# Optimization experiments

Hardware: AMD Instinct MI355X
Metric: run time of the kernel (lower is better)

## Reference

```python
import jax, jax.numpy as jnp
import numpy as np
from jax import lax

NUM_ANCHORS_PER_LEVEL = [196608, 49152, 12288, 3072, 768]
PRE_NMS_TOP_N = 1000
POST_NMS_TOP_N = 1000
NMS_THRESH = 0.7
SCORE_THRESH = 0.0
MIN_SIZE = 0.001
BBOX_XFORM_CLIP = float(np.log(1000.0 / 16.0))
NEG = -1e9


def setup_inputs() -> dict:
    key = jax.random.key(0)
    k1, k2, k3, k4 = jax.random.split(key, 4)
    B = 16
    A = sum(NUM_ANCHORS_PER_LEVEL)
    objectness = jax.random.normal(k1, (B, A), jnp.float32)
    pred_bbox_deltas = jax.random.normal(k2, (B, A, 4), jnp.float32) * 0.1
    cxcy = jax.random.uniform(k3, (A, 2), jnp.float32, 0.0, 1024.0)
    wh = jax.random.uniform(k4, (A, 2), jnp.float32, 16.0, 256.0)
    anchors = jnp.concatenate([cxcy - 0.5 * wh, cxcy + 0.5 * wh], axis=1)
    return {"objectness": objectness, "pred_bbox_deltas": pred_bbox_deltas,
            "anchors": anchors, "image_h": 1024, "image_w": 1024}


def _decode(deltas, anchors):
    # torchvision BoxCoder.decode_single with weights (1,1,1,1)
    # deltas [B, A, 4], anchors [A, 4] -> proposals [B, A, 4] (x1,y1,x2,y2)
    w = anchors[:, 2] - anchors[:, 0]
    h = anchors[:, 3] - anchors[:, 1]
    cx = anchors[:, 0] + 0.5 * w
    cy = anchors[:, 1] + 0.5 * h
    dx, dy = deltas[..., 0], deltas[..., 1]
    dw = jnp.minimum(deltas[..., 2], BBOX_XFORM_CLIP)
    dh = jnp.minimum(deltas[..., 3], BBOX_XFORM_CLIP)
    pcx = dx * w + cx
    pcy = dy * h + cy
    pw = jnp.exp(dw) * w
    ph = jnp.exp(dh) * h
    return jnp.stack([pcx - 0.5 * pw, pcy - 0.5 * ph,
                      pcx + 0.5 * pw, pcy + 0.5 * ph], axis=-1)


def _get_top_n_idx(obj):
    # per-level topk with global offsets, static level sizes -> static shapes
    r, off = [], 0
    for n in NUM_ANCHORS_PER_LEVEL:
        k = min(PRE_NMS_TOP_N, n)
        _, idx = lax.top_k(obj[:, off:off + n], k)
        r.append(idx + off)
        off += n
    return jnp.concatenate(r, axis=1)  # [B, K]


def _nms_keep(boxes, scores, valid):
    # Greedy NMS (torchvision semantics: suppress iou > thresh). Fixed-shape mask version.
    K = boxes.shape[0]
    order = jnp.argsort(-scores)
    b = boxes[order]
    v = valid[order]
    area = jnp.maximum(b[:, 2] - b[:, 0], 0.0) * jnp.maximum(b[:, 3] - b[:, 1], 0.0)
    pos = jnp.arange(K)

    def body(i, keep):
        cur = b[i]
        xx1 = jnp.maximum(cur[0], b[:, 0])
        yy1 = jnp.maximum(cur[1], b[:, 1])
        xx2 = jnp.minimum(cur[2], b[:, 2])
        yy2 = jnp.minimum(cur[3], b[:, 3])
        inter = jnp.maximum(xx2 - xx1, 0.0) * jnp.maximum(yy2 - yy1, 0.0)
        iou = inter / (area[i] + area - inter + 1e-9)
        suppress = (iou > NMS_THRESH) & (pos > i) & keep[i]
        return keep & ~suppress

    keep = lax.fori_loop(0, K, body, v)
    return jnp.zeros(K, bool).at[order].set(keep)


def _process_image(boxes, scores_logit, lvl, img_h, img_w):
    # clip_boxes_to_image
    x1 = jnp.clip(boxes[:, 0], 0.0, img_w)
    y1 = jnp.clip(boxes[:, 1], 0.0, img_h)
    x2 = jnp.clip(boxes[:, 2], 0.0, img_w)
    y2 = jnp.clip(boxes[:, 3], 0.0, img_h)
    boxes = jnp.stack([x1, y1, x2, y2], axis=-1)
    scores = jax.nn.sigmoid(scores_logit)
    ws, hs = x2 - x1, y2 - y1
    valid = (ws >= MIN_SIZE) & (hs >= MIN_SIZE) & (scores >= SCORE_THRESH)
    # batched_nms: offset boxes per level so classes never overlap
    max_coord = jnp.max(boxes)
    offs = lvl.astype(boxes.dtype) * (max_coord + 1.0)
    nms_boxes = boxes + offs[:, None]
    masked = jnp.where(valid, scores, NEG)
    keep = _nms_keep(nms_boxes, masked, valid)
    sel = jnp.where(keep, masked, NEG)
    top_s, top_i = lax.top_k(sel, POST_NMS_TOP_N)
    out_valid = top_s > NEG / 2
    fb = jnp.where(out_valid[:, None], boxes[top_i], 0.0)
    fs = jnp.where(out_valid, top_s, 0.0)
    return fb, fs


def reference(objectness, pred_bbox_deltas, anchors, image_h, image_w):
    proposals = _decode(pred_bbox_deltas, anchors)      # [B, A, 4]
    obj = lax.stop_gradient(objectness)                 # objectness.detach()
    top_idx = _get_top_n_idx(obj)                       # [B, K]
    levels_full = jnp.concatenate([jnp.full((n,), i, jnp.int32)
                                   for i, n in enumerate(NUM_ANCHORS_PER_LEVEL)])
    sel_obj = jnp.take_along_axis(obj, top_idx, axis=1)               # [B, K]
    sel_boxes = jnp.take_along_axis(proposals, top_idx[..., None], axis=1)  # [B, K, 4]
    sel_lvl = levels_full[top_idx]                                    # [B, K]
    fh, fw = float(image_h), float(image_w)
    boxes, scores = jax.vmap(lambda b, s, l: _process_image(b, s, l, fh, fw))(
        sel_boxes, sel_obj, sel_lvl)
    return boxes, scores
```

## Files before the change

### kernel.cpp

```cpp
#include <hip/hip_runtime.h>


#define A_TOTAL 261888
#define B_IMG   16
#define K_TOT   4768
#define NEGV    -1e9f
#define BBOX_CLIP 4.135166556742356f
#define ROWS    1024
#define JOBS_PER_IMG 622
#define TOTAL_JOBS   9952
#define CAPG    4096
#define SL_PER_IMG 18

__constant__ int c_lvl_off[5] = {0, 196608, 245760, 258048, 261120};
__constant__ int c_lvl_n[5]   = {196608, 49152, 12288, 3072, 768};
__constant__ int c_lvl_k[5]   = {1000, 1000, 1000, 1000, 768};
__constant__ int c_sel_off[5] = {0, 1000, 2000, 3000, 4000};

__constant__ int c_s_lvl[SL_PER_IMG]   = {0,0,0,0,0,0,0,0,0,0,0,0, 1,1,1, 2, 3, 4};
__constant__ int c_s_base4[SL_PER_IMG] = {0,4096,8192,12288,16384,20480,24576,28672,
                                          32768,36864,40960,45056, 0,4096,8192, 0, 0, 0};
__constant__ int c_s_len4[SL_PER_IMG]  = {4096,4096,4096,4096,4096,4096,4096,4096,
                                          4096,4096,4096,4096, 4096,4096,4096, 3072, 768, 192};

typedef unsigned long long ull;

__device__ __forceinline__ unsigned fkey(float f) {
    unsigned u = __float_as_uint(f);
    return (u & 0x80000000u) ? ~u : (u | 0x80000000u);
}
__device__ __forceinline__ float inv_fkey(unsigned h) {
    return (h & 0x80000000u) ? __uint_as_float(h ^ 0x80000000u)
                             : __uint_as_float(~h);
}
__device__ __forceinline__ float rlane_f(float v, int l) {
    return __int_as_float(__builtin_amdgcn_readlane(__float_as_int(v), l));
}
__device__ __forceinline__ ull rlane_u64(ull v, int l) {
    int lo = __builtin_amdgcn_readlane((int)(unsigned)v, l);
    int hi = __builtin_amdgcn_readlane((int)(unsigned)(v >> 32), l);
    return ((ull)(unsigned)hi << 32) | (unsigned)lo;
}

__device__ __forceinline__ void bitonic_desc(ull* keys, int S, int tid, int nth) {
    for (int kk = 2; kk <= S; kk <<= 1) {
        for (int jj = kk >> 1; jj > 0; jj >>= 1) {
            for (int i = tid; i < S; i += nth) {
                int ix = i ^ jj;
                if (ix > i) {
                    ull a = keys[i], c = keys[ix];
                    bool desc = ((i & kk) == 0);
                    if (desc ? (a < c) : (a > c)) { keys[i] = c; keys[ix] = a; }
                }
            }
            __syncthreads();
        }
    }
}

__global__ void __launch_bounds__(1024)
init_kernel(unsigned* __restrict__ ghist, int* __restrict__ gcnt,
            ull* __restrict__ growany) {
    const int gid = blockIdx.x * 1024 + threadIdx.x;
    if (gid < 80 * 4096) ghist[gid] = 0u;
    if (gid < 80) gcnt[gid] = 0;
    if (gid < 80 * 16) growany[gid] = 0ull;
}

__global__ void __launch_bounds__(256)
hist_kernel(const float* __restrict__ obj, unsigned* __restrict__ ghist) {
    const int blk = blockIdx.x, b = blk / SL_PER_IMG, r = blk % SL_PER_IMG;
    const int lvl = c_s_lvl[r], base4 = c_s_base4[r], len4 = c_s_len4[r];
    const int g = b * 5 + lvl;
    const int tid = threadIdx.x;
    const float4* src4 = (const float4*)(obj + (size_t)b * A_TOTAL + c_lvl_off[lvl]) + base4;

    __shared__ unsigned lh[2 * 4096];
    for (int i = tid; i < 2 * 4096; i += 256) lh[i] = 0u;
    __syncthreads();
    unsigned* myh = lh + (tid & 1) * 4096;
    for (int i = tid; i < len4; i += 256) {
        float4 v = src4[i];
        atomicAdd(&myh[fkey(v.x) >> 20], 1u);
        atomicAdd(&myh[fkey(v.y) >> 20], 1u);
        atomicAdd(&myh[fkey(v.z) >> 20], 1u);
        atomicAdd(&myh[fkey(v.w) >> 20], 1u);
    }
    __syncthreads();
    for (int bin = tid; bin < 4096; bin += 256) {
        unsigned v = lh[bin] + lh[4096 + bin];
        if (v) atomicAdd(&ghist[g * 4096 + bin], v);
    }
}

__global__ void __launch_bounds__(1024)
thresh_kernel(const unsigned* __restrict__ ghist, unsigned* __restrict__ Tg,
              int* __restrict__ flagg) {
    const int g = blockIdx.x, lvl = g % 5;
    const int n = c_lvl_n[lvl], k = c_lvl_k[lvl];
    const int tid = threadIdx.x;
    if (k >= n) {
        if (tid == 0) { Tg[g] = 0u; flagg[g] = 0; }
        return;
    }
    __shared__ unsigned csum[1024];
    __shared__ int sh_chunk;
    unsigned s = 0;
    for (int q = 0; q < 4; ++q) s += ghist[g * 4096 + tid * 4 + q];
    csum[tid] = s;
    __syncthreads();
    for (int o = 1; o < 1024; o <<= 1) {
        unsigned v = (tid + o < 1024) ? csum[tid + o] : 0u;
        __syncthreads();
        csum[tid] += v;
        __syncthreads();
    }
    if (csum[tid] >= (unsigned)k && (tid == 1023 || csum[tid + 1] < (unsigned)k))
        sh_chunk = tid;
    __syncthreads();
    if (tid == 0) {
        int I = sh_chunk;
        unsigned cum = (I < 1023) ? csum[I + 1] : 0u;
        unsigned bin = 0, cntge = 0;
        for (int c = I * 4 + 3; c >= I * 4; --c) {
            unsigned h = ghist[g * 4096 + c];
            if (cum + h >= (unsigned)k) { bin = (unsigned)c; cntge = cum + h; break; }
            cum += h;
        }
        if (cntge <= CAPG) { Tg[g] = bin << 20; flagg[g] = 0; }
        else               { Tg[g] = 0u;        flagg[g] = 1; }
    }
}

__global__ void __launch_bounds__(256)
collect_kernel(const float* __restrict__ obj, const unsigned* __restrict__ Tg,
               const int* __restrict__ flagg, ull* __restrict__ gkeys,
               int* __restrict__ gcnt) {
    const int blk = blockIdx.x, b = blk / SL_PER_IMG, r = blk % SL_PER_IMG;
    const int lvl = c_s_lvl[r], base4 = c_s_base4[r], len4 = c_s_len4[r];
    const int g = b * 5 + lvl;
    const int tid = threadIdx.x;
    if (flagg[g]) return;
    const unsigned T = Tg[g];
    const float4* src4 = (const float4*)(obj + (size_t)b * A_TOTAL + c_lvl_off[lvl]) + base4;

    __shared__ ull buf[CAPG];
    __shared__ int scnt, sbase;
    if (tid == 0) scnt = 0;
    __syncthreads();
    for (int i = tid; i < len4; i += 256) {
        float4 v = src4[i];
        unsigned u0 = fkey(v.x), u1 = fkey(v.y), u2 = fkey(v.z), u3 = fkey(v.w);
        int al = (base4 + i) << 2;
        if (u0 >= T) { int p = atomicAdd(&scnt, 1); if (p < CAPG) buf[p] = ((ull)u0 << 32) | (unsigned)(~(unsigned)(al + 0)); }
        if (u1 >= T) { int p = atomicAdd(&scnt, 1); if (p < CAPG) buf[p] = ((ull)u1 << 32) | (unsigned)(~(unsigned)(al + 1)); }
        if (u2 >= T) { int p = atomicAdd(&scnt, 1); if (p < CAPG) buf[p] = ((ull)u2 << 32) | (unsigned)(~(unsigned)(al + 2)); }
        if (u3 >= T) { int p = atomicAdd(&scnt, 1); if (p < CAPG) buf[p] = ((ull)u3 << 32) | (unsigned)(~(unsigned)(al + 3)); }
    }
    __syncthreads();
    int c2 = scnt < CAPG ? scnt : CAPG;
    if (tid == 0) sbase = atomicAdd(&gcnt[g], c2);
    __syncthreads();
    for (int j = tid; j < c2; j += 256) {
        int d = sbase + j;
        if (d < CAPG) gkeys[g * CAPG + d] = buf[j];
    }
}

__global__ void __launch_bounds__(1024)
sortgather_kernel(const float* __restrict__ obj, const float* __restrict__ deltas,
                  const float* __restrict__ anchors, const int* __restrict__ ihp,
                  const int* __restrict__ iwp, const unsigned* __restrict__ ghist,
                  const unsigned* __restrict__ Tg, const int* __restrict__ flagg,
                  const ull* __restrict__ gkeys, const int* __restrict__ gcnt,
                  float4* __restrict__ cand_box, float* __restrict__ cand_masked,
                  float* __restrict__ mclvl) {
    const int g = blockIdx.x, b = g / 5, lvl = g % 5;
    const int n = c_lvl_n[lvl], k = c_lvl_k[lvl], off = c_lvl_off[lvl];
    const int so = c_sel_off[lvl];
    const int tid = threadIdx.x;

    __shared__ ull cl[CAPG];
    __shared__ float redf[1024];
    __shared__ unsigned fhist[256];
    __shared__ unsigned csum[1024];
    __shared__ int sh_chunk, sh_rem, sh_cnt;
    __shared__ unsigned sh_bin;

    int cnt;
    if (!flagg[g]) {
        cnt = gcnt[g];
        if (cnt < 0) cnt = 0;
        if (cnt > CAPG) cnt = CAPG;
        for (int i = tid; i < cnt; i += 1024) cl[i] = gkeys[g * CAPG + i];
    } else {
        const float4* src4 = (const float4*)(obj + (size_t)b * A_TOTAL + off);
        const int n4 = n >> 2;
        unsigned s = 0;
        for (int q = 0; q < 4; ++q) s += ghist[g * 4096 + tid * 4 + q];
        csum[tid] = s;
        __syncthreads();
        for (int o = 1; o < 1024; o <<= 1) {
            unsigned v = (tid + o < 1024) ? csum[tid + o] : 0u;
            __syncthreads();
            csum[tid] += v;
            __syncthreads();
        }
        if (csum[tid] >= (unsigned)k && (tid == 1023 || csum[tid + 1] < (unsigned)k))
            sh_chunk = tid;
        __syncthreads();
        if (tid == 0) {
            int I = sh_chunk;
            unsigned cum = (I < 1023) ? csum[I + 1] : 0u;
            for (int c = I * 4 + 3; c >= I * 4; --c) {
                unsigned h = ghist[g * 4096 + c];
                if (cum + h >= (unsigned)k) { sh_bin = (unsigned)c; sh_rem = k - (int)cum; break; }
                cum += h;
            }
        }
        __syncthreads();
        unsigned prefix = sh_bin;
        int rem = sh_rem, done = 12;
        while (done < 32) {
            int w = (32 - done >= 8) ? 8 : (32 - done);
            int shift = 32 - done - w;
            int nb = 1 << w;
            for (int i = tid; i < nb; i += 1024) fhist[i] = 0u;
            __syncthreads();
            for (int i = tid; i < n4; i += 1024) {
                float4 v = src4[i];
                unsigned uu0 = fkey(v.x), uu1 = fkey(v.y), uu2 = fkey(v.z), uu3 = fkey(v.w);
                if ((uu0 >> (shift + w)) == prefix) atomicAdd(&fhist[(uu0 >> shift) & (nb - 1)], 1u);
                if ((uu1 >> (shift + w)) == prefix) atomicAdd(&fhist[(uu1 >> shift) & (nb - 1)], 1u);
                if ((uu2 >> (shift + w)) == prefix) atomicAdd(&fhist[(uu2 >> shift) & (nb - 1)], 1u);
                if ((uu3 >> (shift + w)) == prefix) atomicAdd(&fhist[(uu3 >> shift) & (nb - 1)], 1u);
            }
            __syncthreads();
            if (tid == 0) {
                unsigned cum = 0;
                for (int c = nb - 1; c >= 0; --c) {
                    unsigned h = fhist[c];
                    if (cum + h >= (unsigned)rem) {
                        sh_bin = (prefix << w) | (unsigned)c;
                        sh_rem = rem - (int)cum;
                        break;
                    }
                    cum += h;
                }
            }
            __syncthreads();
            prefix = sh_bin; rem = sh_rem; done += w;
            __syncthreads();
        }
        unsigned T = prefix;
        if (tid == 0) sh_cnt = 0;
        __syncthreads();
        for (int i = tid; i < n4; i += 1024) {
            float4 v = src4[i];
            unsigned u0 = fkey(v.x), u1 = fkey(v.y), u2 = fkey(v.z), u3 = fkey(v.w);
            int base = i << 2;
            if (u0 >= T) { int p = atomicAdd(&sh_cnt, 1); if (p < CAPG) cl[p] = ((ull)u0 << 32) | (unsigned)(~(unsigned)(base + 0)); }
            if (u1 >= T) { int p = atomicAdd(&sh_cnt, 1); if (p < CAPG) cl[p] = ((ull)u1 << 32) | (unsigned)(~(unsigned)(base + 1)); }
            if (u2 >= T) { int p = atomicAdd(&sh_cnt, 1); if (p < CAPG) cl[p] = ((ull)u2 << 32) | (unsigned)(~(unsigned)(base + 2)); }
            if (u3 >= T) { int p = atomicAdd(&sh_cnt, 1); if (p < CAPG) cl[p] = ((ull)u3 << 32) | (unsigned)(~(unsigned)(base + 3)); }
        }
        __syncthreads();
        cnt = sh_cnt; if (cnt > CAPG) cnt = CAPG;
    }

    int S = 1024; while (S < cnt) S <<= 1;
    for (int i = cnt + tid; i < S; i += 1024) cl[i] = 0ull;
    __syncthreads();
    bitonic_desc(cl, S, tid, 1024);

    const float imh = (float)ihp[0];
    const float imw = (float)iwp[0];
    float mx = 0.0f;
    if (tid < k) {
        ull kv = cl[tid];
        unsigned idx = (unsigned)off + (unsigned)(~(unsigned)kv);
        float logit = inv_fkey((unsigned)(kv >> 32));
        float4 anc = ((const float4*)anchors)[idx];
        float w = __fsub_rn(anc.z, anc.x);
        float h = __fsub_rn(anc.w, anc.y);
        float cx = __fadd_rn(anc.x, __fmul_rn(0.5f, w));
        float cy = __fadd_rn(anc.y, __fmul_rn(0.5f, h));
        float4 dl = ((const float4*)deltas)[(size_t)b * A_TOTAL + idx];
        float dx = dl.x, dy = dl.y;
        float dw = fminf(dl.z, BBOX_CLIP);
        float dh = fminf(dl.w, BBOX_CLIP);
        float pcx = __fadd_rn(__fmul_rn(dx, w), cx);
        float pcy = __fadd_rn(__fmul_rn(dy, h), cy);
        float pw = __fmul_rn(expf(dw), w);
        float ph = __fmul_rn(expf(dh), h);
        float x1 = __fsub_rn(pcx, __fmul_rn(0.5f, pw));
        float y1 = __fsub_rn(pcy, __fmul_rn(0.5f, ph));
        float x2 = __fadd_rn(pcx, __fmul_rn(0.5f, pw));
        float y2 = __fadd_rn(pcy, __fmul_rn(0.5f, ph));
        x1 = fminf(fmaxf(x1, 0.0f), imw);
        y1 = fminf(fmaxf(y1, 0.0f), imh);
        x2 = fminf(fmaxf(x2, 0.0f), imw);
        y2 = fminf(fmaxf(y2, 0.0f), imh);
        float score = 1.0f / __fadd_rn(1.0f, expf(-logit));
        bool valid = (__fsub_rn(x2, x1) >= 0.001f) && (__fsub_rn(y2, y1) >= 0.001f);
        cand_box[b * K_TOT + so + tid] = make_float4(x1, y1, x2, y2);
        cand_masked[b * K_TOT + so + tid] = valid ? score : NEGV;
        mx = fmaxf(fmaxf(x1, y1), fmaxf(x2, y2));
    }
    redf[tid] = mx;
    __syncthreads();
    for (int s2 = 512; s2 > 0; s2 >>= 1) {
        if (tid < s2) redf[tid] = fmaxf(redf[tid], redf[tid + s2]);
        __syncthreads();
    }
    if (tid == 0) mclvl[g] = redf[0];
}

__global__ void __launch_bounds__(1024)
sortprep_kernel(const float4* __restrict__ cand_box, const float* __restrict__ cand_masked,
                const float* __restrict__ mclvl,
                float4* __restrict__ sbox, float* __restrict__ sar,
                ull* __restrict__ skeys, ull* __restrict__ svalid) {
    const int g = blockIdx.x, b = g / 5, lvl = g % 5;
    const int n = c_lvl_k[lvl], so = c_sel_off[lvl];
    const int tid = threadIdx.x;
    __shared__ ull keys[1024];
    __shared__ ull sv[16];
    if (tid < 16) sv[tid] = 0ull;
    if (tid < n) {
        float m = cand_masked[b * K_TOT + so + tid];
        keys[tid] = ((ull)fkey(m) << 32) | (unsigned)(~(unsigned)(so + tid));
    } else {
        keys[tid] = 0ull;
    }
    __syncthreads();
    bitonic_desc(keys, 1024, tid, 1024);

    float mc = fmaxf(fmaxf(fmaxf(mclvl[b * 5 + 0], mclvl[b * 5 + 1]),
                           fmaxf(mclvl[b * 5 + 2], mclvl[b * 5 + 3])),
                     mclvl[b * 5 + 4]);
    const float offs = __fmul_rn((float)lvl, __fadd_rn(mc, 1.0f));
    const int r = tid;
    ull kv = keys[r];
    skeys[g * ROWS + r] = kv;
    if (r < n) {
        int slot = (int)(~(unsigned)kv);
        float4 bb = cand_box[b * K_TOT + slot];
        float X1 = __fadd_rn(bb.x, offs);
        float Y1 = __fadd_rn(bb.y, offs);
        float X2 = __fadd_rn(bb.z, offs);
        float Y2 = __fadd_rn(bb.w, offs);
        sbox[g * ROWS + r] = make_float4(X1, Y1, X2, Y2);
        sar[g * ROWS + r] = __fmul_rn(fmaxf(__fsub_rn(X2, X1), 0.0f),
                                      fmaxf(__fsub_rn(Y2, Y1), 0.0f));
        if (inv_fkey((unsigned)(kv >> 32)) <= -1e8f)
            atomicOr(&sv[r >> 6], 1ull << (r & 63));
    } else {
        sbox[g * ROWS + r] = make_float4(0.f, 0.f, 0.f, 0.f);
        sar[g * ROWS + r] = 0.f;
    }
    __syncthreads();
    if (tid < 16) svalid[g * 16 + tid] = sv[tid];
}

__global__ void __launch_bounds__(256)
maskbuild_kernel(const float4* __restrict__ sbox, const float* __restrict__ sar,
                 ull* __restrict__ maskg, ull* __restrict__ growany) {
    const int wave = (blockIdx.x * 256 + threadIdx.x) >> 6;
    const int lane = threadIdx.x & 63;
    if (wave >= TOTAL_JOBS) return;
    const int img = wave / JOBS_PER_IMG;
    int rem = wave - img * JOBS_PER_IMG;
    int lvl, t;
    if (rem >= 544) { lvl = 4; t = rem - 544; }
    else            { lvl = rem / 136; t = rem - lvl * 136; }
    const int g = img * 5 + lvl;
    const int Rp = (c_lvl_k[lvl] + 63) >> 6;
    int rt = 0, tt = t;
    while (tt >= Rp - rt) { tt -= Rp - rt; ++rt; }
    const int ct = rt + tt;
    const int r0 = rt << 6, c0 = ct << 6;

    const float4 rb = sbox[g * ROWS + r0 + lane];
    const float  ra = sar[g * ROWS + r0 + lane];
    const float4 cb = sbox[g * ROWS + c0 + lane];
    const float  ca = sar[g * ROWS + c0 + lane];
    const int row = r0 + lane;

    ull m = 0ull;
    for (int jj = 0; jj < 64; ++jj) {
        float bx1 = rlane_f(cb.x, jj);
        float by1 = rlane_f(cb.y, jj);
        float bx2 = rlane_f(cb.z, jj);
        float by2 = rlane_f(cb.w, jj);
        float aj  = rlane_f(ca, jj);
        float xx1 = fmaxf(rb.x, bx1);
        float yy1 = fmaxf(rb.y, by1);
        float xx2 = fminf(rb.z, bx2);
        float yy2 = fminf(rb.w, by2);
        float inter = __fmul_rn(fmaxf(__fsub_rn(xx2, xx1), 0.0f),
                                fmaxf(__fsub_rn(yy2, yy1), 0.0f));
        float den = __fadd_rn(__fsub_rn(__fadd_rn(ra, aj), inter), 1e-9f);
        float iou = inter / den;
        bool s = (iou > 0.7f) && (c0 + jj > row);
        m |= ((ull)s) << jj;
    }
    maskg[(size_t)(g * 16 + ct) * ROWS + row] = m;
    ull ab = __ballot(m != 0ull);
    if (lane == 0 && ab)
        atomicOr(&growany[g * 16 + rt], ab);
}

__global__ void __launch_bounds__(1024)
scan_kernel(const ull* __restrict__ maskg, const ull* __restrict__ growany,
            const ull* __restrict__ svalid, const ull* __restrict__ skeys,
            ull* __restrict__ klist, int* __restrict__ kcount) {
    const int g = blockIdx.x, lvl = g % 5;
    const int n = c_lvl_k[lvl];
    const int Rp = (n + 63) >> 6;
    const int tid = threadIdx.x;

    __shared__ ull lmask[1024 * 17];
    __shared__ ull lsk[1024];

    if (tid < n) {
        ull rw = growany[g * 16 + (tid >> 6)];
        if ((rw >> (tid & 63)) & 1ull) {
            #pragma unroll 16
            for (int w = 0; w < 16; ++w) {
                ull v = (w < Rp) ? maskg[(size_t)(g * 16 + w) * ROWS + tid] : 0ull;
                lmask[tid * 17 + w] = v;
            }
        }
        lsk[tid] = skeys[g * ROWS + tid];
    }
    __syncthreads();
    if (tid >= 16) return;

    const int lane = tid;
    ull remv_l = svalid[g * 16 + lane];
    ull rany_l = growany[g * 16 + lane];
    ull kpv = 0ull;
    for (int W = 0; W < Rp; ++W) {
        const int base = W << 6;
        const int lim = (n - base >= 64) ? 64 : (n - base);
        const ull wmask = (lim >= 64) ? ~0ull : ((1ull << lim) - 1ull);
        ull curw = rlane_u64(remv_l, W);
        ull heavy = rlane_u64(rany_l, W) & wmask;
        while (heavy) {
            const int j = __ffsll((long long)heavy) - 1;
            heavy &= heavy - 1;
            if (!((curw >> j) & 1ull)) {
                ull mrow = lmask[(base + j) * 17 + lane];
                remv_l |= mrow;
                curw |= rlane_u64(mrow, W);
            }
        }
        kpv = (lane == W) ? (~curw & wmask) : kpv;
    }

    int myc = __popcll(kpv);
    int pos = 0, tot = 0;
    for (int w2 = 0; w2 < 16; ++w2) {
        int c = __builtin_amdgcn_readlane(myc, w2);
        pos += (w2 < lane) ? c : 0;
        tot += c;
    }
    if (lane == 0) kcount[g] = tot;
    ull kw = kpv;
    while (kw) {
        int bit = __ffsll((long long)kw) - 1;
        kw &= kw - 1;
        klist[g * ROWS + pos] = lsk[(lane << 6) + bit];
        ++pos;
    }
}

__global__ void __launch_bounds__(1024)
final_kernel(const float4* __restrict__ cand_box, const ull* __restrict__ klist,
             const int* __restrict__ kcount, float* __restrict__ out) {
    const int img = blockIdx.x >> 2, chunk = blockIdx.x & 3;
    const int tid = threadIdx.x;
    __shared__ ull keys[K_TOT];
    __shared__ int base[6];
    if (tid == 0) {
        int s = 0;
        for (int l = 0; l < 5; ++l) { base[l] = s; s += kcount[img * 5 + l]; }
        base[5] = s;
    }
    __syncthreads();
    const int total = base[5];
    for (int l = 0; l < 5; ++l) {
        int cnt = base[l + 1] - base[l];
        for (int j = tid; j < cnt; j += 1024)
            keys[base[l] + j] = klist[(img * 5 + l) * ROWS + j];
    }
    __syncthreads();

    float* boxes_out = out;
    float* scores_out = out + B_IMG * 1000 * 4;

    for (int i = chunk * 1024 + tid; i < total; i += 4096) {
        int L = 0;
        while (i >= base[L + 1]) ++L;
        ull x = keys[i];
        int grank = i - base[L];
        #pragma unroll
        for (int M = 0; M < 5; ++M) {
            if (M == L) continue;
            int lo = base[M], hi = base[M + 1];
            while (lo < hi) {
                int mid = (lo + hi) >> 1;
                if (keys[mid] > x) lo = mid + 1; else hi = mid;
            }
            grank += lo - base[M];
        }
        if (grank < 1000) {
            int slot = (int)(~(unsigned)x);
            float4 bb = cand_box[img * K_TOT + slot];
            ((float4*)boxes_out)[img * 1000 + grank] = bb;
            scores_out[img * 1000 + grank] = inv_fkey((unsigned)(x >> 32));
        }
    }
    if (chunk == 0) {
        for (int r = total + tid; r < 1000; r += 1024) {
            ((float4*)boxes_out)[img * 1000 + r] = make_float4(0.f, 0.f, 0.f, 0.f);
            scores_out[img * 1000 + r] = 0.f;
        }
    }
}

extern "C" void kernel_launch(void* const* d_in, const int* in_sizes, int n_in,
                              void* d_out, int out_size, void* d_ws, size_t ws_size,
                              hipStream_t stream) {
    const float* obj = (const float*)d_in[0];
    const float* deltas = (const float*)d_in[1];
    const float* anchors = (const float*)d_in[2];
    const int* ih = (const int*)d_in[3];
    const int* iw = (const int*)d_in[4];
    float* out = (float*)d_out;

    char* p = (char*)d_ws;
    float4* cand_box = (float4*)p;   p += (size_t)B_IMG * K_TOT * sizeof(float4);
    float4* sbox = (float4*)p;       p += (size_t)80 * ROWS * sizeof(float4);
    char* upool = p;                 p += (size_t)80 * 16 * ROWS * sizeof(ull);
    ull* maskg = (ull*)upool;
    ull* gkeys = (ull*)upool;
    unsigned* ghist = (unsigned*)(upool + (size_t)80 * CAPG * sizeof(ull));
    ull* svalid = (ull*)p;           p += (size_t)80 * 16 * sizeof(ull);
    ull* growany = (ull*)p;          p += (size_t)80 * 16 * sizeof(ull);
    ull* skeys = (ull*)p;            p += (size_t)80 * ROWS * sizeof(ull);
    ull* klist = (ull*)p;            p += (size_t)80 * ROWS * sizeof(ull);
    float* cand_masked = (float*)p;  p += (size_t)B_IMG * K_TOT * sizeof(float);
    float* sar = (float*)p;          p += (size_t)80 * ROWS * sizeof(float);
    int* kcount = (int*)p;           p += 512;
    float* mclvl = (float*)p;        p += 512;
    unsigned* Tg = (unsigned*)p;     p += 512;
    int* flagg = (int*)p;            p += 512;
    int* gcnt = (int*)p;             p += 512;

    hipLaunchKernelGGL(init_kernel, dim3(320), dim3(1024), 0, stream,
                       ghist, gcnt, growany);
    hipLaunchKernelGGL(hist_kernel, dim3(B_IMG * SL_PER_IMG), dim3(256), 0, stream,
                       obj, ghist);
    hipLaunchKernelGGL(thresh_kernel, dim3(80), dim3(1024), 0, stream,
                       ghist, Tg, flagg);
    hipLaunchKernelGGL(collect_kernel, dim3(B_IMG * SL_PER_IMG), dim3(256), 0, stream,
                       obj, Tg, flagg, gkeys, gcnt);
    hipLaunchKernelGGL(sortgather_kernel, dim3(80), dim3(1024), 0, stream,
                       obj, deltas, anchors, ih, iw, ghist, Tg, flagg, gkeys, gcnt,
                       cand_box, cand_masked, mclvl);
    hipLaunchKernelGGL(sortprep_kernel, dim3(80), dim3(1024), 0, stream,
                       cand_box, cand_masked, mclvl, sbox, sar, skeys, svalid);
    hipLaunchKernelGGL(maskbuild_kernel, dim3(TOTAL_JOBS / 4), dim3(256), 0, stream,
                       sbox, sar, maskg, growany);
    hipLaunchKernelGGL(scan_kernel, dim3(80), dim3(1024), 0, stream,
                       maskg, growany, svalid, skeys, klist, kcount);
    hipLaunchKernelGGL(final_kernel, dim3(64), dim3(1024), 0, stream,
                       cand_box, klist, kcount, out);
}
```

Baseline: 158.7 us.

## Replace global histogram atomics with per-slice histograms and drop init kernel

Each histogram block now writes its own per-slice 4096-bin histogram with plain stores, and the threshold kernel sums the slices per level in shared memory and writes a summed histogram for later use. This removes the init kernel launch and the global atomics, moving zeroing of gcnt and growany into existing kernels. The mask-build kernel also loads column boxes into LDS instead of broadcasting them with readlane, at the cost of a block barrier. The extra slice reads in the threshold kernel add some global traffic.

```diff
diff --git a/kernel.cpp b/kernel.cpp
--- a/kernel.cpp
+++ b/kernel.cpp
@@ -16,6 +16,8 @@
 __constant__ int c_lvl_n[5]   = {196608, 49152, 12288, 3072, 768};
 __constant__ int c_lvl_k[5]   = {1000, 1000, 1000, 1000, 768};
 __constant__ int c_sel_off[5] = {0, 1000, 2000, 3000, 4000};
+__constant__ int c_lvl_sst[5] = {0, 12, 15, 16, 17};
+__constant__ int c_lvl_scn[5] = {12, 3, 1, 1, 1};
 
 __constant__ int c_s_lvl[SL_PER_IMG]   = {0,0,0,0,0,0,0,0,0,0,0,0, 1,1,1, 2, 3, 4};
 __constant__ int c_s_base4[SL_PER_IMG] = {0,4096,8192,12288,16384,20480,24576,28672,
@@ -32,9 +34,6 @@
 __device__ __forceinline__ float inv_fkey(unsigned h) {
     return (h & 0x80000000u) ? __uint_as_float(h ^ 0x80000000u)
                              : __uint_as_float(~h);
-}
-__device__ __forceinline__ float rlane_f(float v, int l) {
-    return __int_as_float(__builtin_amdgcn_readlane(__float_as_int(v), l));
 }
 __device__ __forceinline__ ull rlane_u64(ull v, int l) {
     int lo = __builtin_amdgcn_readlane((int)(unsigned)v, l);
@@ -58,20 +57,10 @@
     }
 }
 
-__global__ void __launch_bounds__(1024)
-init_kernel(unsigned* __restrict__ ghist, int* __restrict__ gcnt,
-            ull* __restrict__ growany) {
-    const int gid = blockIdx.x * 1024 + threadIdx.x;
-    if (gid < 80 * 4096) ghist[gid] = 0u;
-    if (gid < 80) gcnt[gid] = 0;
-    if (gid < 80 * 16) growany[gid] = 0ull;
-}
-
 __global__ void __launch_bounds__(256)
-hist_kernel(const float* __restrict__ obj, unsigned* __restrict__ ghist) {
+hist_kernel(const float* __restrict__ obj, unsigned* __restrict__ phist) {
     const int blk = blockIdx.x, b = blk / SL_PER_IMG, r = blk % SL_PER_IMG;
     const int lvl = c_s_lvl[r], base4 = c_s_base4[r], len4 = c_s_len4[r];
-    const int g = b * 5 + lvl;
     const int tid = threadIdx.x;
     const float4* src4 = (const float4*)(obj + (size_t)b * A_TOTAL + c_lvl_off[lvl]) + base4;
 
@@ -87,26 +76,36 @@
         atomicAdd(&myh[fkey(v.w) >> 20], 1u);
     }
     __syncthreads();
-    for (int bin = tid; bin < 4096; bin += 256) {
-        unsigned v = lh[bin] + lh[4096 + bin];
-        if (v) atomicAdd(&ghist[g * 4096 + bin], v);
-    }
+    for (int bin = tid; bin < 4096; bin += 256)
+        phist[(size_t)blk * 4096 + bin] = lh[bin] + lh[4096 + bin];
 }
 
 __global__ void __launch_bounds__(1024)
-thresh_kernel(const unsigned* __restrict__ ghist, unsigned* __restrict__ Tg,
-              int* __restrict__ flagg) {
-    const int g = blockIdx.x, lvl = g % 5;
+thresh_kernel(const unsigned* __restrict__ phist, unsigned* __restrict__ sghist,
+              unsigned* __restrict__ Tg, int* __restrict__ flagg,
+              int* __restrict__ gcnt) {
+    const int g = blockIdx.x, b = g / 5, lvl = g % 5;
     const int n = c_lvl_n[lvl], k = c_lvl_k[lvl];
     const int tid = threadIdx.x;
+    if (tid == 0) gcnt[g] = 0;
     if (k >= n) {
         if (tid == 0) { Tg[g] = 0u; flagg[g] = 0; }
         return;
     }
+    const int sst = b * SL_PER_IMG + c_lvl_sst[lvl], scn = c_lvl_scn[lvl];
     __shared__ unsigned csum[1024];
     __shared__ int sh_chunk;
+    __shared__ unsigned hist4[4096];
     unsigned s = 0;
-    for (int q = 0; q < 4; ++q) s += ghist[g * 4096 + tid * 4 + q];
+    for (int q = 0; q < 4; ++q) {
+        const int bin = tid * 4 + q;
+        unsigned v = 0;
+        for (int s2 = 0; s2 < scn; ++s2)
+            v += phist[(size_t)(sst + s2) * 4096 + bin];
+        hist4[bin] = v;
+        sghist[g * 4096 + bin] = v;
+        s += v;
+    }
     csum[tid] = s;
     __syncthreads();
     for (int o = 1; o < 1024; o <<= 1) {
@@ -123,7 +122,7 @@
         unsigned cum = (I < 1023) ? csum[I + 1] : 0u;
         unsigned bin = 0, cntge = 0;
         for (int c = I * 4 + 3; c >= I * 4; --c) {
-            unsigned h = ghist[g * 4096 + c];
+            unsigned h = hist4[c];
             if (cum + h >= (unsigned)k) { bin = (unsigned)c; cntge = cum + h; break; }
             cum += h;
         }
@@ -170,7 +169,7 @@
 __global__ void __launch_bounds__(1024)
 sortgather_kernel(const float* __restrict__ obj, const float* __restrict__ deltas,
                   const float* __restrict__ anchors, const int* __restrict__ ihp,
-                  const int* __restrict__ iwp, const unsigned* __restrict__ ghist,
+                  const int* __restrict__ iwp, const unsigned* __restrict__ sghist,
                   const unsigned* __restrict__ Tg, const int* __restrict__ flagg,
                   const ull* __restrict__ gkeys, const int* __restrict__ gcnt,
                   float4* __restrict__ cand_box, float* __restrict__ cand_masked,
@@ -197,7 +196,7 @@
         const float4* src4 = (const float4*)(obj + (size_t)b * A_TOTAL + off);
         const int n4 = n >> 2;
         unsigned s = 0;
-        for (int q = 0; q < 4; ++q) s += ghist[g * 4096 + tid * 4 + q];
+        for (int q = 0; q < 4; ++q) s += sghist[g * 4096 + tid * 4 + q];
         csum[tid] = s;
         __syncthreads();
         for (int o = 1; o < 1024; o <<= 1) {
@@ -213,7 +212,7 @@
             int I = sh_chunk;
             unsigned cum = (I < 1023) ? csum[I + 1] : 0u;
             for (int c = I * 4 + 3; c >= I * 4; --c) {
-                unsigned h = ghist[g * 4096 + c];
+                unsigned h = sghist[g * 4096 + c];
                 if (cum + h >= (unsigned)k) { sh_bin = (unsigned)c; sh_rem = k - (int)cum; break; }
                 cum += h;
             }
@@ -320,13 +319,14 @@
 sortprep_kernel(const float4* __restrict__ cand_box, const float* __restrict__ cand_masked,
                 const float* __restrict__ mclvl,
                 float4* __restrict__ sbox, float* __restrict__ sar,
-                ull* __restrict__ skeys, ull* __restrict__ svalid) {
+                ull* __restrict__ skeys, ull* __restrict__ svalid,
+                ull* __restrict__ growany) {
     const int g = blockIdx.x, b = g / 5, lvl = g % 5;
     const int n = c_lvl_k[lvl], so = c_sel_off[lvl];
     const int tid = threadIdx.x;
     __shared__ ull keys[1024];
     __shared__ ull sv[16];
-    if (tid < 16) sv[tid] = 0ull;
+    if (tid < 16) { sv[tid] = 0ull; growany[g * 16 + tid] = 0ull; }
     if (tid < n) {
         float m = cand_masked[b * K_TOT + so + tid];
         keys[tid] = ((ull)fkey(m) << 32) | (unsigned)(~(unsigned)(so + tid));
@@ -368,7 +368,9 @@
                  ull* __restrict__ maskg, ull* __restrict__ growany) {
     const int wave = (blockIdx.x * 256 + threadIdx.x) >> 6;
     const int lane = threadIdx.x & 63;
-    if (wave >= TOTAL_JOBS) return;
+    const int wv = threadIdx.x >> 6;
+    __shared__ float4 scb[256];
+    __shared__ float sca2[256];
     const int img = wave / JOBS_PER_IMG;
     int rem = wave - img * JOBS_PER_IMG;
     int lvl, t;
@@ -383,21 +385,19 @@
 
     const float4 rb = sbox[g * ROWS + r0 + lane];
     const float  ra = sar[g * ROWS + r0 + lane];
-    const float4 cb = sbox[g * ROWS + c0 + lane];
-    const float  ca = sar[g * ROWS + c0 + lane];
+    scb[threadIdx.x]  = sbox[g * ROWS + c0 + lane];
+    sca2[threadIdx.x] = sar[g * ROWS + c0 + lane];
+    __syncthreads();
     const int row = r0 + lane;
 
     ull m = 0ull;
     for (int jj = 0; jj < 64; ++jj) {
-        float bx1 = rlane_f(cb.x, jj);
-        float by1 = rlane_f(cb.y, jj);
-        float bx2 = rlane_f(cb.z, jj);
-        float by2 = rlane_f(cb.w, jj);
-        float aj  = rlane_f(ca, jj);
-        float xx1 = fmaxf(rb.x, bx1);
-        float yy1 = fmaxf(rb.y, by1);
-        float xx2 = fminf(rb.z, bx2);
-        float yy2 = fminf(rb.w, by2);
+        float4 cbj = scb[(wv << 6) | jj];
+        float aj   = sca2[(wv << 6) | jj];
+        float xx1 = fmaxf(rb.x, cbj.x);
+        float yy1 = fmaxf(rb.y, cbj.y);
+        float xx2 = fminf(rb.z, cbj.z);
+        float yy2 = fminf(rb.w, cbj.w);
         float inter = __fmul_rn(fmaxf(__fsub_rn(xx2, xx1), 0.0f),
                                 fmaxf(__fsub_rn(yy2, yy1), 0.0f));
         float den = __fadd_rn(__fsub_rn(__fadd_rn(ra, aj), inter), 1e-9f);
@@ -546,7 +546,9 @@
     char* upool = p;                 p += (size_t)80 * 16 * ROWS * sizeof(ull);
     ull* maskg = (ull*)upool;
     ull* gkeys = (ull*)upool;
-    unsigned* ghist = (unsigned*)(upool + (size_t)80 * CAPG * sizeof(ull));
+    unsigned* phist = (unsigned*)(upool + (size_t)80 * CAPG * sizeof(ull));
+    unsigned* sghist = (unsigned*)(upool + (size_t)80 * CAPG * sizeof(ull)
+                                   + (size_t)288 * 4096 * sizeof(unsigned));
     ull* svalid = (ull*)p;           p += (size_t)80 * 16 * sizeof(ull);
     ull* growany = (ull*)p;          p += (size_t)80 * 16 * sizeof(ull);
     ull* skeys = (ull*)p;            p += (size_t)80 * ROWS * sizeof(ull);
@@ -559,19 +561,17 @@
     int* flagg = (int*)p;            p += 512;
     int* gcnt = (int*)p;             p += 512;
 
-    hipLaunchKernelGGL(init_kernel, dim3(320), dim3(1024), 0, stream,
-                       ghist, gcnt, growany);
     hipLaunchKernelGGL(hist_kernel, dim3(B_IMG * SL_PER_IMG), dim3(256), 0, stream,
-                       obj, ghist);
+                       obj, phist);
     hipLaunchKernelGGL(thresh_kernel, dim3(80), dim3(1024), 0, stream,
-                       ghist, Tg, flagg);
+                       phist, sghist, Tg, flagg, gcnt);
     hipLaunchKernelGGL(collect_kernel, dim3(B_IMG * SL_PER_IMG), dim3(256), 0, stream,
                        obj, Tg, flagg, gkeys, gcnt);
     hipLaunchKernelGGL(sortgather_kernel, dim3(80), dim3(1024), 0, stream,
-                       obj, deltas, anchors, ih, iw, ghist, Tg, flagg, gkeys, gcnt,
+                       obj, deltas, anchors, ih, iw, sghist, Tg, flagg, gkeys, gcnt,
                        cand_box, cand_masked, mclvl);
     hipLaunchKernelGGL(sortprep_kernel, dim3(80), dim3(1024), 0, stream,
-                       cand_box, cand_masked, mclvl, sbox, sar, skeys, svalid);
+                       cand_box, cand_masked, mclvl, sbox, sar, skeys, svalid, growany);
     hipLaunchKernelGGL(maskbuild_kernel, dim3(TOTAL_JOBS / 4), dim3(256), 0, stream,
                        sbox, sar, maskg, growany);
     hipLaunchKernelGGL(scan_kernel, dim3(80), dim3(1024), 0, stream,
```

After: 149.7 us. 1.06x faster.
